# Kernel optimization log

Hardware: AMD Instinct MI355X
Metric: run time of the kernel (lower is better)

Reference implementation:

```python
import jax, jax.numpy as jnp
import numpy as np

HIDDEN = 2048
NUM_HEADS = 8
NUM_KV_HEADS = 1
HEAD_DIM = 256
ROPE_THETA = 10000.0
B, S = 2, 2048


def setup_inputs() -> dict:
    key = jax.random.key(0)
    k1, k2, k3, k4, k5 = jax.random.split(key, 5)
    scale = 0.02
    hidden_states = jax.random.normal(k1, (B, S, HIDDEN), dtype=jnp.float32)
    Wq = jax.random.normal(k2, (HIDDEN, NUM_HEADS * HEAD_DIM), dtype=jnp.float32) * scale
    Wk = jax.random.normal(k3, (HIDDEN, NUM_KV_HEADS * HEAD_DIM), dtype=jnp.float32) * scale
    Wv = jax.random.normal(k4, (HIDDEN, NUM_KV_HEADS * HEAD_DIM), dtype=jnp.float32) * scale
    Wo = jax.random.normal(k5, (NUM_HEADS * HEAD_DIM, HIDDEN), dtype=jnp.float32) * scale
    # causal mask: 1 = attend, 0 = masked (module adds -1e9 where mask==0)
    attention_mask = jnp.tril(jnp.ones((S, S), dtype=jnp.int32))[None, None].repeat(B, axis=0)
    position_ids = jnp.arange(S, dtype=jnp.int32)[None, :].repeat(B, axis=0)
    return {"hidden_states": hidden_states, "Wq": Wq, "Wk": Wk, "Wv": Wv,
            "Wo": Wo, "attention_mask": attention_mask, "position_ids": position_ids}


def _rotate_half(x):
    half = x.shape[-1] // 2
    return jnp.concatenate([-x[..., half:], x[..., :half]], axis=-1)


def _rope_cos_sin(position_ids, head_dim, theta):
    inv_freq = 1.0 / (theta ** (jnp.arange(0, head_dim, 2, dtype=jnp.float32) / head_dim))
    freqs = position_ids.astype(jnp.float32)[:, :, None] * inv_freq[None, None, :]  # [B,S,D/2]
    emb = jnp.concatenate([freqs, freqs], axis=-1)  # [B,S,D]
    return jnp.cos(emb)[:, None], jnp.sin(emb)[:, None]  # [B,1,S,D]


def reference(hidden_states, Wq, Wk, Wv, Wo, attention_mask, position_ids):
    bsz, q_len, _ = hidden_states.shape
    q = (hidden_states @ Wq).reshape(bsz, q_len, NUM_HEADS, HEAD_DIM).transpose(0, 2, 1, 3)
    k = (hidden_states @ Wk).reshape(bsz, q_len, NUM_KV_HEADS, HEAD_DIM).transpose(0, 2, 1, 3)
    v = (hidden_states @ Wv).reshape(bsz, q_len, NUM_KV_HEADS, HEAD_DIM).transpose(0, 2, 1, 3)
    q = q / jnp.sqrt(jnp.float32(HEAD_DIM))  # scale before RoPE, as in source
    cos, sin = _rope_cos_sin(position_ids, HEAD_DIM, ROPE_THETA)
    q = q * cos + _rotate_half(q) * sin
    k = k * cos + _rotate_half(k) * sin
    # GQA: repeat kv heads (prefill: cache == current k,v)
    groups = NUM_HEADS // NUM_KV_HEADS
    k = jnp.repeat(k, groups, axis=1)
    v = jnp.repeat(v, groups, axis=1)
    attn = jnp.einsum('bhqd,bhkd->bhqk', q, k)  # [B,H,S,S]
    additive = jnp.where(attention_mask == 0, jnp.float32(-1e9), jnp.float32(0.0))
    attn = jax.nn.softmax(attn + additive, axis=-1)
    out = jnp.einsum('bhqk,bhkd->bhqd', attn, v)
    out = out.transpose(0, 2, 1, 3).reshape(bsz, q_len, NUM_HEADS * HEAD_DIM)
    out = out @ Wo
    return out, attn
```

## Files before the change

kernel.cpp:

```cpp
#include <hip/hip_runtime.h>

typedef __bf16 bf16_t;
typedef __attribute__((ext_vector_type(4))) float f32x4;
typedef __attribute__((ext_vector_type(8))) __bf16 bf16x8;
typedef __attribute__((ext_vector_type(4))) __bf16 bf16x4;

#define DEVI __device__ __forceinline__

static constexpr int kBsz = 2, kS = 2048, kH = 8, kD = 256, kHid = 2048, kNqkv = 2560;

DEVI void gload_lds16(const void* g, void* l) {
  __builtin_amdgcn_global_load_lds(
      (__attribute__((address_space(1))) unsigned int*)g,
      (__attribute__((address_space(3))) unsigned int*)l, 16, 0, 0);
}

__global__ __launch_bounds__(256) void cast_f32_bf16(const float* __restrict__ in,
                                                     bf16_t* __restrict__ out) {
  int idx = blockIdx.x * 256 + threadIdx.x;
  const float4 f = ((const float4*)in)[idx];
  bf16x4 o;
  o[0] = (bf16_t)f.x; o[1] = (bf16_t)f.y; o[2] = (bf16_t)f.z; o[3] = (bf16_t)f.w;
  ((bf16x4*)out)[idx] = o;
}

__global__ void wtrans_all(const float* __restrict__ Wq, const float* __restrict__ Wk,
                           const float* __restrict__ Wv, const float* __restrict__ Wo,
                           bf16_t* __restrict__ WqkvT, bf16_t* __restrict__ WoT) {
  __shared__ float tile[32][33];
  int zb = blockIdx.x;
  const float* src;
  bf16_t* dst;
  int C, bx, by;
  if (zb < 4096) {
    src = Wq; dst = WqkvT; C = 2048; bx = zb & 63; by = zb >> 6;
  } else if (zb < 4608) {
    int u = zb - 4096; src = Wk; dst = WqkvT + (size_t)2048 * 2048; C = 256; bx = u & 7; by = u >> 3;
  } else if (zb < 5120) {
    int u = zb - 4608; src = Wv; dst = WqkvT + (size_t)2304 * 2048; C = 256; bx = u & 7; by = u >> 3;
  } else {
    int u = zb - 5120; src = Wo; dst = WoT; C = 2048; bx = u & 63; by = u >> 6;
  }
  int c0 = bx * 32, r0 = by * 32;
  int tx = threadIdx.x, ty = threadIdx.y;
#pragma unroll
  for (int k = 0; k < 4; k++)
    tile[ty + 8 * k][tx] = src[(size_t)(r0 + ty + 8 * k) * C + c0 + tx];
  __syncthreads();
#pragma unroll
  for (int k = 0; k < 4; k++)
    dst[(size_t)(c0 + ty + 8 * k) * 2048 + r0 + tx] = (bf16_t)tile[tx][ty + 8 * k];
}

__global__ __launch_bounds__(256) void transpose_v(const bf16_t* __restrict__ qkv,
                                                   bf16_t* __restrict__ vT) {
  __shared__ float tile[32][33];
  int d0 = blockIdx.x * 32, s0 = blockIdx.y * 32, b = blockIdx.z;
  int tx = threadIdx.x, ty = threadIdx.y;
  const bf16_t* in = qkv + ((size_t)(b * kS + s0)) * kNqkv + 2304 + d0;
#pragma unroll
  for (int k = 0; k < 4; k++)
    tile[ty + 8 * k][tx] = (float)in[(size_t)(ty + 8 * k) * kNqkv + tx];
  __syncthreads();
  bf16_t* out = vT + ((size_t)(b * kD + d0)) * kS + s0;
#pragma unroll
  for (int k = 0; k < 4; k++)
    out[(size_t)(ty + 8 * k) * kS + tx] = (bf16_t)tile[tx][ty + 8 * k];
}

__global__ __launch_bounds__(256) void rope_all(const bf16_t* __restrict__ qkv,
                                                const int* __restrict__ pos_ids,
                                                bf16_t* __restrict__ q_bh,
                                                bf16_t* __restrict__ k_b) {
  int bid = blockIdx.x;
  if (bid < 16384) {
    int idx = bid * 256 + threadIdx.x;
    int j = idx & 127, s = (idx >> 7) & 2047, h = (idx >> 18) & 7, b = idx >> 21;
    float invf = exp2f(-0.103810253f * (float)j);
    float ang = (float)pos_ids[b * kS + s] * invf;
    float c, sn;
    sincosf(ang, &sn, &c);
    const bf16_t* src = qkv + ((size_t)(b * kS + s)) * kNqkv + h * kD;
    float x0 = (float)src[j] * 0.0625f;
    float x1 = (float)src[j + 128] * 0.0625f;
    bf16_t* dst = q_bh + ((size_t)((b * kH + h) * kS + s)) * kD;
    dst[j] = (bf16_t)(x0 * c - x1 * sn);
    dst[j + 128] = (bf16_t)(x1 * c + x0 * sn);
  } else {
    int idx = (bid - 16384) * 256 + threadIdx.x;
    int j = idx & 127, s = (idx >> 7) & 2047, b = idx >> 18;
    float invf = exp2f(-0.103810253f * (float)j);
    float ang = (float)pos_ids[b * kS + s] * invf;
    float c, sn;
    sincosf(ang, &sn, &c);
    const bf16_t* src = qkv + ((size_t)(b * kS + s)) * kNqkv + 2048;
    float x0 = (float)src[j];
    float x1 = (float)src[j + 128];
    bf16_t* dst = k_b + ((size_t)(b * kS + s)) * kD;
    dst[j] = (bf16_t)(x0 * c - x1 * sn);
    dst[j + 128] = (bf16_t)(x1 * c + x0 * sn);
  }
}

__global__ __launch_bounds__(256) void attn_fused(
    const bf16_t* __restrict__ q_bh, const bf16_t* __restrict__ k_b,
    float* __restrict__ attn, bf16_t* __restrict__ P) {
  constexpr int LDK = 264;
  __shared__ bf16_t ks[128 * LDK];
  __shared__ float lstat[64][2][16];
  __shared__ float rowinv[64];
  const int lin = blockIdx.y * 32 + blockIdx.x;
  const int xr = (lin >> 1) & 31;
  const int flip = (lin ^ (lin >> 8)) & 1;
  const int rt = flip ? 31 - xr : xr;
  const int z = (lin & 1) | (((lin >> 6) & 7) << 1);
  const int b = z >> 3;
  const int dkt = rt >> 1, nkt = dkt + 1;
  const int m0 = rt * 64;
  const int t = threadIdx.x, lane = t & 63, wv = t >> 6;
  const int wm2 = (wv & 1) * 32, wn2 = (wv >> 1) * 64, wc = wv >> 1;
  const int lrow = lane & 15, quad = lane >> 4;

  bf16x8 qf[2][8];
  {
    const bf16_t* qb = q_bh + ((size_t)z * kS + m0) * kD;
#pragma unroll
    for (int mi = 0; mi < 2; mi++)
#pragma unroll
      for (int k8 = 0; k8 < 8; k8++)
        qf[mi][k8] = *(const bf16x8*)(qb + (size_t)(wm2 + mi * 16 + lrow) * kD + k8 * 32 + quad * 8);
  }
  const bf16_t* kb = k_b + (size_t)b * kS * kD;

  for (int kt = 0; kt < nkt; kt++) {
    __syncthreads();
    bf16x8 stg[8];
#pragma unroll
    for (int half = 0; half < 2; half++) {
#pragma unroll
      for (int it = 0; it < 8; it++) {
        int f = (half * 8 + it) * 256 + t, r = f >> 5, c = f & 31;
        stg[it] = *(const bf16x8*)(kb + (size_t)(kt * 128 + r) * kD + c * 8);
      }
#pragma unroll
      for (int it = 0; it < 8; it++) {
        int f = (half * 8 + it) * 256 + t, r = f >> 5, c = f & 31;
        *(bf16x8*)(ks + r * LDK + c * 8) = stg[it];
      }
    }
    __syncthreads();
    f32x4 acc[2][4];
#pragma unroll
    for (int mi = 0; mi < 2; mi++)
#pragma unroll
      for (int ni = 0; ni < 4; ni++) acc[mi][ni] = f32x4{0.f, 0.f, 0.f, 0.f};
    __builtin_amdgcn_s_setprio(1);
#pragma unroll
    for (int k8 = 0; k8 < 8; k8++) {
      bf16x8 bfv[4];
#pragma unroll
      for (int ni = 0; ni < 4; ni++)
        bfv[ni] = *(const bf16x8*)(ks + (wn2 + ni * 16 + lrow) * LDK + k8 * 32 + quad * 8);
#pragma unroll
      for (int mi = 0; mi < 2; mi++)
#pragma unroll
        for (int ni = 0; ni < 4; ni++)
          acc[mi][ni] = __builtin_amdgcn_mfma_f32_16x16x32_bf16(qf[mi][k8], bfv[ni], acc[mi][ni], 0, 0, 0);
    }
    __builtin_amdgcn_s_setprio(0);
    const bool diag = (kt == dkt);
#pragma unroll
    for (int mi = 0; mi < 2; mi++)
#pragma unroll
      for (int rr = 0; rr < 4; rr++) {
        int ml = wm2 + mi * 16 + quad * 4 + rr;
        int mg = m0 + ml;
        float s4 = 0.f;
#pragma unroll
        for (int ni = 0; ni < 4; ni++) {
          int ng = kt * 128 + wn2 + ni * 16 + lrow;
          float e = __expf(fminf(acc[mi][ni][rr], 80.f));
          s4 += (!diag || ng <= mg) ? e : 0.f;
        }
        s4 += __shfl_xor(s4, 1); s4 += __shfl_xor(s4, 2);
        s4 += __shfl_xor(s4, 4); s4 += __shfl_xor(s4, 8);
        if (lrow == 0) lstat[ml][wc][kt] = s4;
      }
  }
  __syncthreads();
  if (t < 64) {
    float l = 0.f;
    for (int j = 0; j < nkt; j++) l += lstat[t][0][j] + lstat[t][1][j];
    rowinv[t] = 1.f / l;
  }
  __syncthreads();

  float* arow = attn + ((size_t)z * kS + m0) * kS;
  bf16_t* prow = P + ((size_t)z * kS + m0) * kS;
  for (int kt = 0; kt < nkt; kt++) {
    __syncthreads();
    bf16x8 stg[8];
#pragma unroll
    for (int half = 0; half < 2; half++) {
#pragma unroll
      for (int it = 0; it < 8; it++) {
        int f = (half * 8 + it) * 256 + t, r = f >> 5, c = f & 31;
        stg[it] = *(const bf16x8*)(kb + (size_t)(kt * 128 + r) * kD + c * 8);
      }
#pragma unroll
      for (int it = 0; it < 8; it++) {
        int f = (half * 8 + it) * 256 + t, r = f >> 5, c = f & 31;
        *(bf16x8*)(ks + r * LDK + c * 8) = stg[it];
      }
    }
    __syncthreads();
    f32x4 acc[2][4];
#pragma unroll
    for (int mi = 0; mi < 2; mi++)
#pragma unroll
      for (int ni = 0; ni < 4; ni++) acc[mi][ni] = f32x4{0.f, 0.f, 0.f, 0.f};
    __builtin_amdgcn_s_setprio(1);
#pragma unroll
    for (int k8 = 0; k8 < 8; k8++) {
      bf16x8 bfv[4];
#pragma unroll
      for (int ni = 0; ni < 4; ni++)
        bfv[ni] = *(const bf16x8*)(ks + (wn2 + ni * 16 + lrow) * LDK + k8 * 32 + quad * 8);
#pragma unroll
      for (int mi = 0; mi < 2; mi++)
#pragma unroll
        for (int ni = 0; ni < 4; ni++)
          acc[mi][ni] = __builtin_amdgcn_mfma_f32_16x16x32_bf16(qf[mi][k8], bfv[ni], acc[mi][ni], 0, 0, 0);
    }
    __builtin_amdgcn_s_setprio(0);
    const bool diag = (kt == dkt);
#pragma unroll
    for (int mi = 0; mi < 2; mi++)
#pragma unroll
      for (int rr = 0; rr < 4; rr++) {
        int ml = wm2 + mi * 16 + quad * 4 + rr;
        int mg = m0 + ml;
        float inv = rowinv[ml];
        float* ap = arow + (size_t)ml * kS + kt * 128;
        bf16_t* pp = prow + (size_t)ml * kS + kt * 128;
#pragma unroll
        for (int ni = 0; ni < 4; ni++) {
          int nl = wn2 + ni * 16 + lrow;
          int ng = kt * 128 + nl;
          float e = __expf(fminf(acc[mi][ni][rr], 80.f)) * inv;
          float pv = (!diag || ng <= mg) ? e : 0.f;
          ap[nl] = pv;
          pp[nl] = (bf16_t)pv;
        }
      }
  }
  int c0 = nkt * 128;
  int nf4 = (kS - c0) >> 2;
  for (int rr = 0; rr < 64; rr++) {
    float* ap = arow + (size_t)rr * kS + c0;
    for (int cc = t; cc < nf4; cc += 256)
      *(float4*)(ap + cc * 4) = make_float4(0.f, 0.f, 0.f, 0.f);
  }
}

template <int OUT, int CKTR, int BAL = 0>
__global__ __launch_bounds__(256) void gemm_bt(
    const bf16_t* __restrict__ Av, const bf16_t* __restrict__ Btv, void* __restrict__ Cv,
    int K, int lda, int ldb, int ldc,
    long long aBatch, long long bBatch, int bzShift, long long cBatch) {
  constexpr int BM = 128, BN = 128, BK = 32;
  __shared__ bf16_t As[BM * BK];
  __shared__ bf16_t Bs[BN * BK];
  const int z = blockIdx.z;
  const int n0 = blockIdx.x * BN;
  int byi = blockIdx.y;
  if (BAL) {
    if ((blockIdx.x ^ (blockIdx.z >> 3)) & 1) byi = gridDim.y - 1 - byi;
  }
  const int m0 = byi * BM;
  const bf16_t* Bt = Btv + (size_t)(z >> bzShift) * bBatch + (size_t)n0 * ldb;
  const int kEnd = CKTR ? ((m0 + BM < K) ? (m0 + BM) : K) : K;
  const int t = threadIdx.x;
  const int lane = t & 63, wv = t >> 6;
  const int wm = (wv & 1) << 6, wn = (wv >> 1) << 6;
  const int lrow = lane & 15, quad = lane >> 4;
  f32x4 zero = {0.f, 0.f, 0.f, 0.f};
  f32x4 acc[4][4];
#pragma unroll
  for (int i = 0; i < 4; i++)
#pragma unroll
    for (int j = 0; j < 4; j++) acc[i][j] = zero;

  const bf16_t* Ab = Av + (size_t)z * aBatch + (size_t)m0 * lda;

  for (int k0 = 0; k0 < kEnd; k0 += BK) {
    __syncthreads();
    {
      const bf16_t* ga = Ab + (size_t)(t >> 2) * lda + k0 + (t & 3) * 8;
      gload_lds16(ga, As + t * 8);
      gload_lds16(ga + (size_t)64 * lda, As + 2048 + t * 8);
    }
    {
      const bf16_t* gb = Bt + (size_t)(t >> 2) * ldb + k0 + (t & 3) * 8;
      gload_lds16(gb, Bs + t * 8);
      gload_lds16(gb + (size_t)64 * ldb, Bs + 2048 + t * 8);
    }
    __syncthreads();
    bf16x8 af[4], bfv[4];
#pragma unroll
    for (int i = 0; i < 4; i++)
      af[i] = *(const bf16x8*)(As + (wm + i * 16 + lrow) * BK + quad * 8);
#pragma unroll
    for (int i = 0; i < 4; i++)
      bfv[i] = *(const bf16x8*)(Bs + (wn + i * 16 + lrow) * BK + quad * 8);
#pragma unroll
    for (int mi = 0; mi < 4; mi++)
#pragma unroll
      for (int ni = 0; ni < 4; ni++)
        acc[mi][ni] = __builtin_amdgcn_mfma_f32_16x16x32_bf16(af[mi], bfv[ni], acc[mi][ni], 0, 0, 0);
  }

  if (OUT == 0) {
    float* C = (float*)Cv + (size_t)z * cBatch;
#pragma unroll
    for (int mi = 0; mi < 4; mi++) {
      int m = m0 + wm + mi * 16 + quad * 4;
#pragma unroll
      for (int ni = 0; ni < 4; ni++) {
        int n = n0 + wn + ni * 16 + lrow;
#pragma unroll
        for (int r = 0; r < 4; r++) C[(size_t)(m + r) * ldc + n] = acc[mi][ni][r];
      }
    }
  } else if (OUT == 1) {
    bf16_t* C = (bf16_t*)Cv + (size_t)(z >> 3) * cBatch + (size_t)(z & 7) * kD;
#pragma unroll
    for (int mi = 0; mi < 4; mi++) {
      int m = m0 + wm + mi * 16 + quad * 4;
#pragma unroll
      for (int ni = 0; ni < 4; ni++) {
        int n = n0 + wn + ni * 16 + lrow;
#pragma unroll
        for (int r = 0; r < 4; r++) C[(size_t)(m + r) * ldc + n] = (bf16_t)acc[mi][ni][r];
      }
    }
  } else {
    bf16_t* C = (bf16_t*)Cv + (size_t)z * cBatch;
#pragma unroll
    for (int mi = 0; mi < 4; mi++) {
      int m = m0 + wm + mi * 16 + quad * 4;
#pragma unroll
      for (int ni = 0; ni < 4; ni++) {
        int n = n0 + wn + ni * 16 + lrow;
#pragma unroll
        for (int r = 0; r < 4; r++) C[(size_t)(m + r) * ldc + n] = (bf16_t)acc[mi][ni][r];
      }
    }
  }
}

extern "C" void kernel_launch(void* const* d_in, const int* in_sizes, int n_in,
                              void* d_out, int out_size, void* d_ws, size_t ws_size,
                              hipStream_t stream) {
  const float* hs = (const float*)d_in[0];
  const float* Wq = (const float*)d_in[1];
  const float* Wk = (const float*)d_in[2];
  const float* Wv = (const float*)d_in[3];
  const float* Wo = (const float*)d_in[4];
  const int* pos = (const int*)d_in[6];

  float* out = (float*)d_out;
  float* attn = out + (size_t)kBsz * kS * kHid;

  char* w = (char*)d_ws;
  bf16_t* hsb = (bf16_t*)w;   w += (size_t)4096 * 2048 * 2;
  bf16_t* WqkvT = (bf16_t*)w; w += (size_t)2560 * 2048 * 2;
  bf16_t* WoT = (bf16_t*)w;   w += (size_t)2048 * 2048 * 2;
  bf16_t* qkv = (bf16_t*)w;   w += (size_t)4096 * 2560 * 2;
  bf16_t* q_bh = (bf16_t*)w;  w += (size_t)8388608 * 2;
  bf16_t* k_b = (bf16_t*)w;   w += (size_t)1048576 * 2;
  bf16_t* vT = (bf16_t*)w;    w += (size_t)1048576 * 2;
  bf16_t* av = (bf16_t*)w;    w += (size_t)8388608 * 2;
  bf16_t* Pb = (bf16_t*)w;    w += (size_t)16 * 2048 * 2048 * 2;

  cast_f32_bf16<<<8192, 256, 0, stream>>>(hs, hsb);
  wtrans_all<<<9216, dim3(32, 8), 0, stream>>>(Wq, Wk, Wv, Wo, WqkvT, WoT);

  gemm_bt<2, 0><<<dim3(20, 32, 1), 256, 0, stream>>>(
      hsb, WqkvT, qkv, 2048, 2048, 2048, 2560, 0, 0, 0, 0);

  rope_all<<<18432, 256, 0, stream>>>(qkv, pos, q_bh, k_b);
  transpose_v<<<dim3(8, 64, 2), dim3(32, 8), 0, stream>>>(qkv, vT);

  attn_fused<<<dim3(32, 16), 256, 0, stream>>>(q_bh, k_b, attn, Pb);

  gemm_bt<1, 1, 1><<<dim3(2, 16, 16), 256, 0, stream>>>(
      Pb, vT, av, 2048, 2048, 2048, 2048,
      (long long)4194304, (long long)524288, 3, (long long)(kS * kHid));

  gemm_bt<0, 0><<<dim3(16, 32, 1), 256, 0, stream>>>(
      av, WoT, out, 2048, 2048, 2048, 2048, 0, 0, 0, 0);
}
```

Baseline: 741.0 us.

## Shrink attention K tile to 64 with swizzled direct LDS loads; widen GEMM BK

The fused attention kernel now stages 64-row K tiles into shared memory through direct global-to-LDS loads using an XOR swizzle instead of padded rows, and sets launch bounds for higher occupancy. It also keeps per-thread running row sums in registers rather than writing per-tile partials to shared memory, and adds explicit zeroing of the P tail for even row tiles because of the finer causal granularity. The GEMM's K step doubles to 64 with two MFMA sub-steps per stage, halving its barrier count. These changes trade more tile iterations in attention for less LDS use and more resident blocks, with some added correctness risk around the P zero fill.

```diff
diff --git a/kernel.cpp b/kernel.cpp
--- a/kernel.cpp
+++ b/kernel.cpp
@@ -102,12 +102,12 @@
   }
 }
 
-__global__ __launch_bounds__(256) void attn_fused(
+__global__ __launch_bounds__(256, 4) void attn_fused(
     const bf16_t* __restrict__ q_bh, const bf16_t* __restrict__ k_b,
     float* __restrict__ attn, bf16_t* __restrict__ P) {
-  constexpr int LDK = 264;
-  __shared__ bf16_t ks[128 * LDK];
-  __shared__ float lstat[64][2][16];
+  constexpr int KT = 64;
+  __shared__ bf16_t ks[KT * 256];
+  __shared__ float lstat[64][2];
   __shared__ float rowinv[64];
   const int lin = blockIdx.y * 32 + blockIdx.x;
   const int xr = (lin >> 1) & 31;
@@ -115,10 +115,10 @@
   const int rt = flip ? 31 - xr : xr;
   const int z = (lin & 1) | (((lin >> 6) & 7) << 1);
   const int b = z >> 3;
-  const int dkt = rt >> 1, nkt = dkt + 1;
+  const int nkt = rt + 1, dkt = rt;
   const int m0 = rt * 64;
   const int t = threadIdx.x, lane = t & 63, wv = t >> 6;
-  const int wm2 = (wv & 1) * 32, wn2 = (wv >> 1) * 64, wc = wv >> 1;
+  const int wm2 = (wv & 1) * 32, wn2 = (wv >> 1) * 32, wc = wv >> 1;
   const int lrow = lane & 15, quad = lane >> 4;
 
   bf16x8 qf[2][8];
@@ -132,39 +132,41 @@
   }
   const bf16_t* kb = k_b + (size_t)b * kS * kD;
 
+  float rs[2][4];
+#pragma unroll
+  for (int mi = 0; mi < 2; mi++)
+#pragma unroll
+    for (int rr = 0; rr < 4; rr++) rs[mi][rr] = 0.f;
+
   for (int kt = 0; kt < nkt; kt++) {
     __syncthreads();
-    bf16x8 stg[8];
-#pragma unroll
-    for (int half = 0; half < 2; half++) {
-#pragma unroll
-      for (int it = 0; it < 8; it++) {
-        int f = (half * 8 + it) * 256 + t, r = f >> 5, c = f & 31;
-        stg[it] = *(const bf16x8*)(kb + (size_t)(kt * 128 + r) * kD + c * 8);
-      }
-#pragma unroll
-      for (int it = 0; it < 8; it++) {
-        int f = (half * 8 + it) * 256 + t, r = f >> 5, c = f & 31;
-        *(bf16x8*)(ks + r * LDK + c * 8) = stg[it];
-      }
-    }
-    __syncthreads();
-    f32x4 acc[2][4];
+#pragma unroll
+    for (int i = 0; i < 8; i++) {
+      int slot = i * 256 + t;
+      int r = slot >> 5;
+      int c = (slot & 31) ^ (r & 7);
+      gload_lds16(kb + (size_t)(kt * KT + r) * kD + c * 8, ks + slot * 8);
+    }
+    __syncthreads();
+    f32x4 acc[2][2];
 #pragma unroll
     for (int mi = 0; mi < 2; mi++)
 #pragma unroll
-      for (int ni = 0; ni < 4; ni++) acc[mi][ni] = f32x4{0.f, 0.f, 0.f, 0.f};
+      for (int ni = 0; ni < 2; ni++) acc[mi][ni] = f32x4{0.f, 0.f, 0.f, 0.f};
     __builtin_amdgcn_s_setprio(1);
 #pragma unroll
     for (int k8 = 0; k8 < 8; k8++) {
-      bf16x8 bfv[4];
-#pragma unroll
-      for (int ni = 0; ni < 4; ni++)
-        bfv[ni] = *(const bf16x8*)(ks + (wn2 + ni * 16 + lrow) * LDK + k8 * 32 + quad * 8);
+      bf16x8 bfv[2];
+#pragma unroll
+      for (int ni = 0; ni < 2; ni++) {
+        int R = wn2 + ni * 16 + lrow;
+        int c16 = (k8 * 4 + quad) ^ (R & 7);
+        bfv[ni] = *(const bf16x8*)(ks + R * 256 + c16 * 8);
+      }
 #pragma unroll
       for (int mi = 0; mi < 2; mi++)
 #pragma unroll
-        for (int ni = 0; ni < 4; ni++)
+        for (int ni = 0; ni < 2; ni++)
           acc[mi][ni] = __builtin_amdgcn_mfma_f32_16x16x32_bf16(qf[mi][k8], bfv[ni], acc[mi][ni], 0, 0, 0);
     }
     __builtin_amdgcn_s_setprio(0);
@@ -175,61 +177,57 @@
       for (int rr = 0; rr < 4; rr++) {
         int ml = wm2 + mi * 16 + quad * 4 + rr;
         int mg = m0 + ml;
-        float s4 = 0.f;
-#pragma unroll
-        for (int ni = 0; ni < 4; ni++) {
-          int ng = kt * 128 + wn2 + ni * 16 + lrow;
+#pragma unroll
+        for (int ni = 0; ni < 2; ni++) {
+          int ng = kt * KT + wn2 + ni * 16 + lrow;
           float e = __expf(fminf(acc[mi][ni][rr], 80.f));
-          s4 += (!diag || ng <= mg) ? e : 0.f;
+          rs[mi][rr] += (!diag || ng <= mg) ? e : 0.f;
         }
-        s4 += __shfl_xor(s4, 1); s4 += __shfl_xor(s4, 2);
-        s4 += __shfl_xor(s4, 4); s4 += __shfl_xor(s4, 8);
-        if (lrow == 0) lstat[ml][wc][kt] = s4;
-      }
-  }
+      }
+  }
+#pragma unroll
+  for (int mi = 0; mi < 2; mi++)
+#pragma unroll
+    for (int rr = 0; rr < 4; rr++) {
+      float s4 = rs[mi][rr];
+      s4 += __shfl_xor(s4, 1); s4 += __shfl_xor(s4, 2);
+      s4 += __shfl_xor(s4, 4); s4 += __shfl_xor(s4, 8);
+      if (lrow == 0) lstat[wm2 + mi * 16 + quad * 4 + rr][wc] = s4;
+    }
   __syncthreads();
-  if (t < 64) {
-    float l = 0.f;
-    for (int j = 0; j < nkt; j++) l += lstat[t][0][j] + lstat[t][1][j];
-    rowinv[t] = 1.f / l;
-  }
-  __syncthreads();
+  if (t < 64) rowinv[t] = 1.f / (lstat[t][0] + lstat[t][1]);
 
   float* arow = attn + ((size_t)z * kS + m0) * kS;
   bf16_t* prow = P + ((size_t)z * kS + m0) * kS;
   for (int kt = 0; kt < nkt; kt++) {
     __syncthreads();
-    bf16x8 stg[8];
-#pragma unroll
-    for (int half = 0; half < 2; half++) {
-#pragma unroll
-      for (int it = 0; it < 8; it++) {
-        int f = (half * 8 + it) * 256 + t, r = f >> 5, c = f & 31;
-        stg[it] = *(const bf16x8*)(kb + (size_t)(kt * 128 + r) * kD + c * 8);
-      }
-#pragma unroll
-      for (int it = 0; it < 8; it++) {
-        int f = (half * 8 + it) * 256 + t, r = f >> 5, c = f & 31;
-        *(bf16x8*)(ks + r * LDK + c * 8) = stg[it];
-      }
-    }
-    __syncthreads();
-    f32x4 acc[2][4];
+#pragma unroll
+    for (int i = 0; i < 8; i++) {
+      int slot = i * 256 + t;
+      int r = slot >> 5;
+      int c = (slot & 31) ^ (r & 7);
+      gload_lds16(kb + (size_t)(kt * KT + r) * kD + c * 8, ks + slot * 8);
+    }
+    __syncthreads();
+    f32x4 acc[2][2];
 #pragma unroll
     for (int mi = 0; mi < 2; mi++)
 #pragma unroll
-      for (int ni = 0; ni < 4; ni++) acc[mi][ni] = f32x4{0.f, 0.f, 0.f, 0.f};
+      for (int ni = 0; ni < 2; ni++) acc[mi][ni] = f32x4{0.f, 0.f, 0.f, 0.f};
     __builtin_amdgcn_s_setprio(1);
 #pragma unroll
     for (int k8 = 0; k8 < 8; k8++) {
-      bf16x8 bfv[4];
-#pragma unroll
-      for (int ni = 0; ni < 4; ni++)
-        bfv[ni] = *(const bf16x8*)(ks + (wn2 + ni * 16 + lrow) * LDK + k8 * 32 + quad * 8);
+      bf16x8 bfv[2];
+#pragma unroll
+      for (int ni = 0; ni < 2; ni++) {
+        int R = wn2 + ni * 16 + lrow;
+        int c16 = (k8 * 4 + quad) ^ (R & 7);
+        bfv[ni] = *(const bf16x8*)(ks + R * 256 + c16 * 8);
+      }
 #pragma unroll
       for (int mi = 0; mi < 2; mi++)
 #pragma unroll
-        for (int ni = 0; ni < 4; ni++)
+        for (int ni = 0; ni < 2; ni++)
           acc[mi][ni] = __builtin_amdgcn_mfma_f32_16x16x32_bf16(qf[mi][k8], bfv[ni], acc[mi][ni], 0, 0, 0);
     }
     __builtin_amdgcn_s_setprio(0);
@@ -241,12 +239,12 @@
         int ml = wm2 + mi * 16 + quad * 4 + rr;
         int mg = m0 + ml;
         float inv = rowinv[ml];
-        float* ap = arow + (size_t)ml * kS + kt * 128;
-        bf16_t* pp = prow + (size_t)ml * kS + kt * 128;
-#pragma unroll
-        for (int ni = 0; ni < 4; ni++) {
+        float* ap = arow + (size_t)ml * kS + kt * KT;
+        bf16_t* pp = prow + (size_t)ml * kS + kt * KT;
+#pragma unroll
+        for (int ni = 0; ni < 2; ni++) {
           int nl = wn2 + ni * 16 + lrow;
-          int ng = kt * 128 + nl;
+          int ng = kt * KT + nl;
           float e = __expf(fminf(acc[mi][ni][rr], 80.f)) * inv;
           float pv = (!diag || ng <= mg) ? e : 0.f;
           ap[nl] = pv;
@@ -254,13 +252,21 @@
         }
       }
   }
-  int c0 = nkt * 128;
+  int c0 = nkt * KT;
   int nf4 = (kS - c0) >> 2;
   for (int rr = 0; rr < 64; rr++) {
     float* ap = arow + (size_t)rr * kS + c0;
     for (int cc = t; cc < nf4; cc += 256)
       *(float4*)(ap + cc * 4) = make_float4(0.f, 0.f, 0.f, 0.f);
   }
+  if ((rt & 1) == 0) {
+    int pc0 = nkt * KT;
+    int r = t >> 2, cchunk = (t & 3) * 16;
+    bf16x8 zz = {(bf16_t)0.f, (bf16_t)0.f, (bf16_t)0.f, (bf16_t)0.f,
+                 (bf16_t)0.f, (bf16_t)0.f, (bf16_t)0.f, (bf16_t)0.f};
+    *(bf16x8*)(prow + (size_t)r * kS + pc0 + cchunk) = zz;
+    *(bf16x8*)(prow + (size_t)r * kS + pc0 + cchunk + 8) = zz;
+  }
 }
 
 template <int OUT, int CKTR, int BAL = 0>
@@ -268,7 +274,7 @@
     const bf16_t* __restrict__ Av, const bf16_t* __restrict__ Btv, void* __restrict__ Cv,
     int K, int lda, int ldb, int ldc,
     long long aBatch, long long bBatch, int bzShift, long long cBatch) {
-  constexpr int BM = 128, BN = 128, BK = 32;
+  constexpr int BM = 128, BN = 128, BK = 64;
   __shared__ bf16_t As[BM * BK];
   __shared__ bf16_t Bs[BN * BK];
   const int z = blockIdx.z;
@@ -295,29 +301,34 @@
 
   for (int k0 = 0; k0 < kEnd; k0 += BK) {
     __syncthreads();
-    {
-      const bf16_t* ga = Ab + (size_t)(t >> 2) * lda + k0 + (t & 3) * 8;
-      gload_lds16(ga, As + t * 8);
-      gload_lds16(ga + (size_t)64 * lda, As + 2048 + t * 8);
-    }
-    {
-      const bf16_t* gb = Bt + (size_t)(t >> 2) * ldb + k0 + (t & 3) * 8;
-      gload_lds16(gb, Bs + t * 8);
-      gload_lds16(gb + (size_t)64 * ldb, Bs + 2048 + t * 8);
-    }
-    __syncthreads();
-    bf16x8 af[4], bfv[4];
-#pragma unroll
-    for (int i = 0; i < 4; i++)
-      af[i] = *(const bf16x8*)(As + (wm + i * 16 + lrow) * BK + quad * 8);
-#pragma unroll
-    for (int i = 0; i < 4; i++)
-      bfv[i] = *(const bf16x8*)(Bs + (wn + i * 16 + lrow) * BK + quad * 8);
-#pragma unroll
-    for (int mi = 0; mi < 4; mi++)
-#pragma unroll
-      for (int ni = 0; ni < 4; ni++)
-        acc[mi][ni] = __builtin_amdgcn_mfma_f32_16x16x32_bf16(af[mi], bfv[ni], acc[mi][ni], 0, 0, 0);
+#pragma unroll
+    for (int i = 0; i < 4; i++) {
+      int slot = i * 256 + t;
+      int r = slot >> 3, c = slot & 7;
+      gload_lds16(Ab + (size_t)r * lda + k0 + c * 8, As + slot * 8);
+    }
+#pragma unroll
+    for (int i = 0; i < 4; i++) {
+      int slot = i * 256 + t;
+      int r = slot >> 3, c = slot & 7;
+      gload_lds16(Bt + (size_t)r * ldb + k0 + c * 8, Bs + slot * 8);
+    }
+    __syncthreads();
+#pragma unroll
+    for (int k8 = 0; k8 < 2; k8++) {
+      bf16x8 af[4], bfv[4];
+#pragma unroll
+      for (int i = 0; i < 4; i++)
+        af[i] = *(const bf16x8*)(As + (wm + i * 16 + lrow) * BK + k8 * 32 + quad * 8);
+#pragma unroll
+      for (int i = 0; i < 4; i++)
+        bfv[i] = *(const bf16x8*)(Bs + (wn + i * 16 + lrow) * BK + k8 * 32 + quad * 8);
+#pragma unroll
+      for (int mi = 0; mi < 4; mi++)
+#pragma unroll
+        for (int ni = 0; ni < 4; ni++)
+          acc[mi][ni] = __builtin_amdgcn_mfma_f32_16x16x32_bf16(af[mi], bfv[ni], acc[mi][ni], 0, 0, 0);
+    }
   }
 
   if (OUT == 0) {
```

Result: no change. 742.1 us (+0.1%).
